# Kernel tuning notes

Measured on AMD Instinct MI355X. Metric: run time of the kernel, lower is better.

The kernel has to match this reference:

```python
import jax, jax.numpy as jnp
import numpy as np

B, L, H, O, N = 64, 2048, 128, 128, 256  # batch, window, num_states, num_actions, dynamics state dim


def setup_inputs() -> dict:
    key = jax.random.key(0)
    ks = jax.random.split(key, 12)
    # LRU-style stable init: |lambda| in (r_min, r_max)
    u1 = jax.random.uniform(ks[0], (N,))
    u2 = jax.random.uniform(ks[1], (N,))
    r_min, r_max = 0.4, 0.99
    nu_log = jnp.log(-0.5 * jnp.log(u1 * (r_max**2 - r_min**2) + r_min**2))
    theta_log = jnp.log(u2 * 2.0 * jnp.pi)
    lam_abs2 = jnp.exp(-2.0 * jnp.exp(nu_log))
    gamma_log = 0.5 * jnp.log(1.0 - lam_abs2)  # gamma normalization
    return {
        "state": jax.random.normal(ks[2], (B, H), jnp.float32),
        "dynamics_input_time_window": jax.random.normal(ks[3], (B, L, H), jnp.float32),
        "dynamics_disturbance_time_window": jax.random.normal(ks[4], (B, L, H), jnp.float32),
        "nu_log": nu_log.astype(jnp.float32),
        "theta_log": theta_log.astype(jnp.float32),
        "gamma_log": gamma_log.astype(jnp.float32),
        "B_re": jax.random.normal(ks[5], (N, H), jnp.float32) / np.sqrt(2 * H),
        "B_im": jax.random.normal(ks[6], (N, H), jnp.float32) / np.sqrt(2 * H),
        "C_re": jax.random.normal(ks[7], (O, N), jnp.float32) / np.sqrt(N),
        "C_im": jax.random.normal(ks[8], (O, N), jnp.float32) / np.sqrt(N),
        "D": jax.random.normal(ks[9], (O, H), jnp.float32) / np.sqrt(H),
    }


def _ssm_scan(u, nu_log, theta_log, gamma_log, B_re, B_im, C_re, C_im, D):
    # u: [B, L, H] real. Diagonal complex LRU: x_t = lam * x_{t-1} + gamma*B u_t; y = Re(C x) + D u
    lam = jnp.exp(-jnp.exp(nu_log) + 1j * jnp.exp(theta_log))           # [N]
    Bmat = (B_re + 1j * B_im) * jnp.exp(gamma_log)[:, None]              # [N, H]
    Bu = jnp.einsum("blh,nh->bln", u.astype(jnp.complex64), Bmat)       # [B, L, N]
    lam_seq = jnp.broadcast_to(lam, Bu.shape)

    def comb(e1, e2):
        a1, b1 = e1
        a2, b2 = e2
        return a1 * a2, a2 * b1 + b2

    _, x = jax.lax.associative_scan(comb, (lam_seq, Bu), axis=1)        # [B, L, N]
    y = jnp.einsum("bln,on->blo", x, C_re + 1j * C_im).real
    y = y + jnp.einsum("blh,oh->blo", u, D)
    return y


def reference(state, dynamics_input_time_window, dynamics_disturbance_time_window,
              nu_log, theta_log, gamma_log, B_re, B_im, C_re, C_im, D):
    # 3-dim branch of Actor.forward: run SSM over the disturbance window, take last step
    y = _ssm_scan(dynamics_disturbance_time_window, nu_log, theta_log, gamma_log,
                  B_re, B_im, C_re, C_im, D)                             # [B, L, O]
    action = y[:, -1, :]                                                 # [B, O]
    return action
```

## Files before the change

### kernel.cpp

```cpp
#include <hip/hip_runtime.h>
#include <hip/hip_bf16.h>
#include <math.h>
#include <stdint.h>

#define B_ 64
#define L_ 2048
#define H_ 128
#define O_ 128
#define N_ 256
#define CH_ 128
#define NCH_ 16
#define SPC_ 8

using f32x4 = __attribute__((ext_vector_type(4))) float;
using i32x4 = __attribute__((ext_vector_type(4))) int;
using i32x2 = __attribute__((ext_vector_type(2))) int;
using h16x8 = __attribute__((ext_vector_type(8))) _Float16;

__device__ __forceinline__ unsigned short f16_bits(float v) {
    _Float16 h = (_Float16)v;
    return __builtin_bit_cast(unsigned short, h);
}
__device__ __forceinline__ int pack_f16(float a, float b) {
    return (int)((unsigned)f16_bits(a) | ((unsigned)f16_bits(b) << 16));
}

__global__ void prep_kernel(const float* __restrict__ nu_log, const float* __restrict__ theta_log,
                            const float* __restrict__ gamma_log, const float* __restrict__ B_re,
                            const float* __restrict__ B_im, unsigned short* __restrict__ B2Tr,
                            float2* __restrict__ lamjR, float2* __restrict__ lam16R,
                            float2* __restrict__ lamCCr, float* __restrict__ nuR,
                            int* __restrict__ perm, float* __restrict__ X) {
    __shared__ float nu_s[N_];
    __shared__ int perm_s[N_];
    const int t = threadIdx.x;
    float nu = expf(nu_log[t]);
    nu_s[t] = nu;
    __syncthreads();
    {
        int rank = 0;
        for (int j = 0; j < N_; ++j) {
            float vj = nu_s[j];
            rank += (vj < nu || (vj == nu && j < t)) ? 1 : 0;
        }
        perm_s[rank] = t;
    }
    __syncthreads();
    const int bb = blockIdx.x;
    if (bb < 64) {
        #pragma unroll
        for (int kk = 0; kk < 4; ++kk) {
            int e = bb * 1024 + kk * 256 + t;
            int part = e >> 15, rank = (e >> 7) & 255, h = e & 127;
            int n = perm_s[rank];
            float g = expf(gamma_log[n]);
            float v = (part ? B_im : B_re)[n * H_ + h] * g;
            B2Tr[e] = f16_bits(v);
        }
    } else if (bb == 64) {
        int r = t, n = perm_s[r];
        float nun = nu_s[n];
        double th = (double)expf(theta_log[n]);
        double rr = exp(-(double)nun);
        double sn, cs;
        sincos(th, &sn, &cs);
        double lre = rr * cs, lim = rr * sn;
        double pre = 1.0, pim = 0.0;
        for (int k = 0; k < 16; ++k) {
            lamjR[r * 16 + 15 - k] = make_float2((float)pre, (float)pim);
            double t1 = pre * lre - pim * lim, t2 = pre * lim + pim * lre;
            pre = t1; pim = t2;
        }
        lam16R[r] = make_float2((float)pre, (float)pim);
        nuR[r] = nun;
        perm[r] = n;
        double wre = pre, wim = pim;
        for (int i = 0; i < 3; ++i) {
            double a = wre * wre - wim * wim, b2 = 2.0 * wre * wim;
            wre = a; wim = b2;
        }
        double are = 1.0, aim = 0.0;
        for (int c = 15; c >= 0; --c) {
            lamCCr[c * N_ + r] = make_float2((float)are, (float)aim);
            double a = are * wre - aim * wim, b2 = are * wim + aim * wre;
            are = a; aim = b2;
        }
    } else {
        int idx = (bb - 65) * 1024 + t * 4;
        f32x4 z = {0.f, 0.f, 0.f, 0.f};
        *(f32x4*)&X[idx] = z;
    }
}

__global__ __launch_bounds__(512, 4)
void scan_kernel(const float* __restrict__ u, const unsigned short* __restrict__ B2Tr,
                 const float2* __restrict__ lamjR, const float2* __restrict__ lam16R,
                 const float2* __restrict__ lamCCr, const float* __restrict__ nuR,
                 const int* __restrict__ perm, float* __restrict__ X) {
    const int bx = blockIdx.x;
    const int c = bx >> 6;
    const int b = bx & 63;
    const int tid = threadIdx.x;

    __shared__ __align__(16) unsigned short Asm[CH_ * H_];

    const float* gsrc = u + ((size_t)b * L_ + (size_t)(c * CH_)) * H_;
    f32x4 Lv[8];
    #pragma unroll
    for (int k = 0; k < 8; ++k)
        Lv[k] = *(const f32x4*)(gsrc + k * 2048 + tid * 4);

    const int g = tid >> 6;
    const int lane = tid & 63;
    const int m = lane & 15, q = lane >> 4;
    const int p0 = g, p1 = 15 - g;
    const float base_e = 2032.0f - 128.0f * (float)c;
    const float nu0 = nuR[p0 * 16];
    const float nu1 = nuR[p1 * 16];
    int spA = (int)ceilf((base_e - 35.0f / nu0) * 0.0625f);
    if (spA < 0) spA = 0;
    int spB = (int)ceilf((base_e - 35.0f / nu1) * 0.0625f);
    if (spB < 0) spB = 0;

    {
        const int c4 = tid & 31;
        const int gg = c4 >> 1;
        const int half = c4 & 1;
        #pragma unroll
        for (int k = 0; k < 8; ++k) {
            const int r = k * 16 + (tid >> 5);
            i32x2 w;
            w[0] = pack_f16(Lv[k][0], Lv[k][1]);
            w[1] = pack_f16(Lv[k][2], Lv[k][3]);
            *(i32x2*)&Asm[r * H_ + ((gg ^ (r & 15)) * 8) + half * 4] = w;
        }
    }
    __syncthreads();

    if (spA < SPC_) {
        #pragma unroll
        for (int p = 0; p < 2; ++p) {
            const int sp = p ? spB : spA;
            if (sp >= SPC_) continue;
            const int pp = p ? p1 : p0;
            const int rank = pp * 16 + m;

            h16x8 bfr[2][4];
            #pragma unroll
            for (int part = 0; part < 2; ++part) {
                const unsigned short* rp = B2Tr + (size_t)(part * N_ + rank) * H_ + q * 8;
                #pragma unroll
                for (int sl = 0; sl < 4; ++sl)
                    bfr[part][sl] = *(const h16x8*)(rp + sl * 32);
            }
            float2 wl[4];
            #pragma unroll
            for (int r2 = 0; r2 < 4; ++r2) wl[r2] = lamjR[rank * 16 + q * 4 + r2];
            const float2 l16 = lam16R[rank];

            float2 zre = make_float2(0.f, 0.f), zim = make_float2(0.f, 0.f);
            for (int s = sp; s < SPC_; ++s) {
                const int row = s * 16 + m;
                h16x8 afr[4];
                #pragma unroll
                for (int sl = 0; sl < 4; ++sl) {
                    const int unit = (sl * 4 + q) ^ m;
                    afr[sl] = *(const h16x8*)&Asm[row * H_ + unit * 8];
                }
                float2 t0 = zre;
                zre.x = l16.x * t0.x - l16.y * t0.y;
                zre.y = l16.x * t0.y + l16.y * t0.x;
                float2 t1 = zim;
                zim.x = l16.x * t1.x - l16.y * t1.y;
                zim.y = l16.x * t1.y + l16.y * t1.x;
                f32x4 acc = {0.f, 0.f, 0.f, 0.f};
                #pragma unroll
                for (int sl = 0; sl < 4; ++sl)
                    acc = __builtin_amdgcn_mfma_f32_16x16x32_f16(afr[sl], bfr[0][sl], acc, 0, 0, 0);
                #pragma unroll
                for (int r2 = 0; r2 < 4; ++r2) {
                    zre.x += wl[r2].x * acc[r2];
                    zre.y += wl[r2].y * acc[r2];
                }
                f32x4 acc2 = {0.f, 0.f, 0.f, 0.f};
                #pragma unroll
                for (int sl = 0; sl < 4; ++sl)
                    acc2 = __builtin_amdgcn_mfma_f32_16x16x32_f16(afr[sl], bfr[1][sl], acc2, 0, 0, 0);
                #pragma unroll
                for (int r2 = 0; r2 < 4; ++r2) {
                    zim.x += wl[r2].x * acc2[r2];
                    zim.y += wl[r2].y * acc2[r2];
                }
            }

            float a = zre.x, b2 = zre.y, c2 = zim.x, d2 = zim.y;
            a  += __shfl_xor(a, 16);  a  += __shfl_xor(a, 32);
            b2 += __shfl_xor(b2, 16); b2 += __shfl_xor(b2, 32);
            c2 += __shfl_xor(c2, 16); c2 += __shfl_xor(c2, 32);
            d2 += __shfl_xor(d2, 16); d2 += __shfl_xor(d2, 32);
            if (lane < 16) {
                const int n = perm[rank];
                float2 lc = lamCCr[c * N_ + rank];
                float prr = lc.x * a - lc.y * b2;
                float pri = lc.x * b2 + lc.y * a;
                float pir = lc.x * c2 - lc.y * d2;
                float pii = lc.x * d2 + lc.y * c2;
                atomicAdd(&X[(size_t)(b * N_ + n) * 2 + 0], prr - pii);
                atomicAdd(&X[(size_t)(b * N_ + n) * 2 + 1], pri + pir);
            }
        }
    }
}

__global__ __launch_bounds__(512)
void out_kernel(const float* __restrict__ X, const float* __restrict__ C_re,
                const float* __restrict__ C_im, const float* __restrict__ Dm,
                const float* __restrict__ u, float* __restrict__ out) {
    __shared__ __align__(16) float xre[N_];
    __shared__ __align__(16) float xim[N_];
    __shared__ __align__(16) float ul[H_];
    const int b = blockIdx.x;
    const int t = threadIdx.x;
    if (t < N_) {
        float2 x2 = *(const float2*)&X[(size_t)(b * N_ + t) * 2];
        xre[t] = x2.x;
        xim[t] = x2.y;
    }
    if (t < H_) ul[t] = u[((size_t)b * L_ + (L_ - 1)) * H_ + t];
    __syncthreads();
    const int o = t >> 2;
    const int part = t & 3;
    const float* cre = C_re + o * N_ + part * 64;
    const float* cim = C_im + o * N_ + part * 64;
    const float* xr  = xre + part * 64;
    const float* xi  = xim + part * 64;
    float s = 0.f;
    #pragma unroll
    for (int i = 0; i < 16; ++i) {
        f32x4 cr = *(const f32x4*)(cre + i * 4);
        f32x4 ci = *(const f32x4*)(cim + i * 4);
        f32x4 vr = *(const f32x4*)(xr + i * 4);
        f32x4 vi = *(const f32x4*)(xi + i * 4);
        s += cr[0] * vr[0] - ci[0] * vi[0];
        s += cr[1] * vr[1] - ci[1] * vi[1];
        s += cr[2] * vr[2] - ci[2] * vi[2];
        s += cr[3] * vr[3] - ci[3] * vi[3];
    }
    const float* dp = Dm + o * H_ + part * 32;
    const float* up = ul + part * 32;
    #pragma unroll
    for (int i = 0; i < 8; ++i) {
        f32x4 d4 = *(const f32x4*)(dp + i * 4);
        f32x4 u4 = *(const f32x4*)(up + i * 4);
        s += d4[0] * u4[0] + d4[1] * u4[1] + d4[2] * u4[2] + d4[3] * u4[3];
    }
    s += __shfl_xor(s, 1);
    s += __shfl_xor(s, 2);
    if (part == 0) out[b * O_ + o] = s;
}

extern "C" void kernel_launch(void* const* d_in, const int* in_sizes, int n_in,
                              void* d_out, int out_size, void* d_ws, size_t ws_size,
                              hipStream_t stream) {
    const float* u         = (const float*)d_in[2];
    const float* nu_log    = (const float*)d_in[3];
    const float* theta_log = (const float*)d_in[4];
    const float* gamma_log = (const float*)d_in[5];
    const float* B_re      = (const float*)d_in[6];
    const float* B_im      = (const float*)d_in[7];
    const float* C_re      = (const float*)d_in[8];
    const float* C_im      = (const float*)d_in[9];
    const float* Dm        = (const float*)d_in[10];

    char* ws = (char*)d_ws;
    float*          X      = (float*)ws;
    unsigned short* B2Tr   = (unsigned short*)(ws + 131072);
    float2*         lamjR  = (float2*)(ws + 262144);
    float2*         lam16R = (float2*)(ws + 294912);
    float2*         lamCCr = (float2*)(ws + 296960);
    float*          nuR    = (float*)(ws + 329728);
    int*            perm   = (int*)(ws + 330752);

    prep_kernel<<<97, 256, 0, stream>>>(nu_log, theta_log, gamma_log, B_re, B_im,
                                        B2Tr, lamjR, lam16R, lamCCr, nuR, perm, X);
    scan_kernel<<<B_ * NCH_, 512, 0, stream>>>(u, B2Tr, lamjR, lam16R, lamCCr, nuR, perm, X);
    out_kernel<<<B_, 512, 0, stream>>>(X, C_re, C_im, Dm, u, (float*)d_out);
}
```

Measured before the change: 172.5 us.

## Split each scan chunk into two half-chunk blocks of 256 threads

The scan kernel now launches twice as many blocks, each handling a 64-step half of a 128-step chunk with 256 threads. Each wave covers four state groups instead of two, and the first half's contribution is scaled by an extra lambda^64 factor before the atomic add. This is meant to raise occupancy and improve load balance, letting more blocks skip work when decay makes their window negligible. In exchange it doubles the number of atomic adds to X and reloads the B fragments once per block.

```diff
diff --git a/kernel.cpp b/kernel.cpp
--- a/kernel.cpp
+++ b/kernel.cpp
@@ -10,7 +10,8 @@
 #define N_ 256
 #define CH_ 128
 #define NCH_ 16
-#define SPC_ 8
+#define HB_ 64
+#define SPH_ 4
 
 using f32x4 = __attribute__((ext_vector_type(4))) float;
 using i32x4 = __attribute__((ext_vector_type(4))) int;
@@ -23,6 +24,9 @@
 }
 __device__ __forceinline__ int pack_f16(float a, float b) {
     return (int)((unsigned)f16_bits(a) | ((unsigned)f16_bits(b) << 16));
+}
+__device__ __forceinline__ float2 cmul(float2 a, float2 b) {
+    return make_float2(a.x * b.x - a.y * b.y, a.x * b.y + a.y * b.x);
 }
 
 __global__ void prep_kernel(const float* __restrict__ nu_log, const float* __restrict__ theta_log,
@@ -92,57 +96,61 @@
     }
 }
 
-__global__ __launch_bounds__(512, 4)
+__global__ __launch_bounds__(256, 8)
 void scan_kernel(const float* __restrict__ u, const unsigned short* __restrict__ B2Tr,
                  const float2* __restrict__ lamjR, const float2* __restrict__ lam16R,
                  const float2* __restrict__ lamCCr, const float* __restrict__ nuR,
                  const int* __restrict__ perm, float* __restrict__ X) {
     const int bx = blockIdx.x;
-    const int c = bx >> 6;
-    const int b = bx & 63;
+    const int ch = bx >> 6;
+    const int b  = bx & 63;
+    const int c  = ch >> 1;
+    const int h  = ch & 1;
     const int tid = threadIdx.x;
 
-    __shared__ __align__(16) unsigned short Asm[CH_ * H_];
-
-    const float* gsrc = u + ((size_t)b * L_ + (size_t)(c * CH_)) * H_;
+    __shared__ __align__(16) unsigned short Asm[HB_ * H_];
+
+    const float* gsrc = u + ((size_t)b * L_ + (size_t)(c * CH_ + h * HB_)) * H_;
     f32x4 Lv[8];
     #pragma unroll
     for (int k = 0; k < 8; ++k)
-        Lv[k] = *(const f32x4*)(gsrc + k * 2048 + tid * 4);
+        Lv[k] = *(const f32x4*)(gsrc + k * 1024 + tid * 4);
 
     const int g = tid >> 6;
     const int lane = tid & 63;
     const int m = lane & 15, q = lane >> 4;
-    const int p0 = g, p1 = 15 - g;
-    const float base_e = 2032.0f - 128.0f * (float)c;
-    const float nu0 = nuR[p0 * 16];
-    const float nu1 = nuR[p1 * 16];
-    int spA = (int)ceilf((base_e - 35.0f / nu0) * 0.0625f);
-    if (spA < 0) spA = 0;
-    int spB = (int)ceilf((base_e - 35.0f / nu1) * 0.0625f);
-    if (spB < 0) spB = 0;
+    const int pid0 = g, pid1 = 7 - g, pid2 = 8 + g, pid3 = 15 - g;
+    const float base_e = 2032.0f - 128.0f * (float)c - 64.0f * (float)h;
+    const float nv0 = nuR[pid0 * 16];
+    const float nv1 = nuR[pid1 * 16];
+    const float nv2 = nuR[pid2 * 16];
+    const float nv3 = nuR[pid3 * 16];
+    int sp0 = (int)ceilf((base_e - 35.0f / nv0) * 0.0625f); if (sp0 < 0) sp0 = 0;
+    int sp1 = (int)ceilf((base_e - 35.0f / nv1) * 0.0625f); if (sp1 < 0) sp1 = 0;
+    int sp2 = (int)ceilf((base_e - 35.0f / nv2) * 0.0625f); if (sp2 < 0) sp2 = 0;
+    int sp3 = (int)ceilf((base_e - 35.0f / nv3) * 0.0625f); if (sp3 < 0) sp3 = 0;
 
     {
         const int c4 = tid & 31;
         const int gg = c4 >> 1;
-        const int half = c4 & 1;
+        const int hl = c4 & 1;
         #pragma unroll
         for (int k = 0; k < 8; ++k) {
-            const int r = k * 16 + (tid >> 5);
+            const int r = k * 8 + (tid >> 5);
             i32x2 w;
             w[0] = pack_f16(Lv[k][0], Lv[k][1]);
             w[1] = pack_f16(Lv[k][2], Lv[k][3]);
-            *(i32x2*)&Asm[r * H_ + ((gg ^ (r & 15)) * 8) + half * 4] = w;
+            *(i32x2*)&Asm[r * H_ + ((gg ^ (r & 15)) * 8) + hl * 4] = w;
         }
     }
     __syncthreads();
 
-    if (spA < SPC_) {
+    if (sp0 < SPH_) {
         #pragma unroll
-        for (int p = 0; p < 2; ++p) {
-            const int sp = p ? spB : spA;
-            if (sp >= SPC_) continue;
-            const int pp = p ? p1 : p0;
+        for (int p = 0; p < 4; ++p) {
+            const int pp = (p == 0) ? pid0 : (p == 1) ? pid1 : (p == 2) ? pid2 : pid3;
+            const int sp = (p == 0) ? sp0 : (p == 1) ? sp1 : (p == 2) ? sp2 : sp3;
+            if (sp >= SPH_) continue;
             const int rank = pp * 16 + m;
 
             h16x8 bfr[2][4];
@@ -159,7 +167,7 @@
             const float2 l16 = lam16R[rank];
 
             float2 zre = make_float2(0.f, 0.f), zim = make_float2(0.f, 0.f);
-            for (int s = sp; s < SPC_; ++s) {
+            for (int s = sp; s < SPH_; ++s) {
                 const int row = s * 16 + m;
                 h16x8 afr[4];
                 #pragma unroll
@@ -201,6 +209,10 @@
             if (lane < 16) {
                 const int n = perm[rank];
                 float2 lc = lamCCr[c * N_ + rank];
+                if (h == 0) {
+                    float2 l32 = cmul(l16, l16);
+                    lc = cmul(lc, cmul(l32, l32));
+                }
                 float prr = lc.x * a - lc.y * b2;
                 float pri = lc.x * b2 + lc.y * a;
                 float pir = lc.x * c2 - lc.y * d2;
@@ -283,6 +295,6 @@
 
     prep_kernel<<<97, 256, 0, stream>>>(nu_log, theta_log, gamma_log, B_re, B_im,
                                         B2Tr, lamjR, lam16R, lamCCr, nuR, perm, X);
-    scan_kernel<<<B_ * NCH_, 512, 0, stream>>>(u, B2Tr, lamjR, lam16R, lamCCr, nuR, perm, X);
+    scan_kernel<<<2048, 256, 0, stream>>>(u, B2Tr, lamjR, lam16R, lamCCr, nuR, perm, X);
     out_kernel<<<B_, 512, 0, stream>>>(X, C_re, C_im, Dm, u, (float*)d_out);
 }
```

Measured after the change: 202.4 us. 1.17x slower.
